# Kernel optimization log

Hardware: AMD Instinct MI355X
Metric: run time of the kernel (lower is better)

The kernel has to match this reference:

```python
import jax, jax.numpy as jnp
import numpy as np

B, S, D, H = 2, 2048, 1024, 16
A = D // H
NEG = -1e9


def setup_inputs() -> dict:
    key = jax.random.key(0)
    ks = jax.random.split(key, 5)
    std = 1.0 / np.sqrt(D)
    query = jax.random.normal(ks[0], (B, S, D), dtype=jnp.float32)
    context = jax.random.normal(ks[1], (B, S, D), dtype=jnp.float32)
    Wq = jax.random.normal(ks[2], (D, D), dtype=jnp.float32) * std
    Wkv = jax.random.normal(ks[3], (2 * D, D), dtype=jnp.float32) * std
    Wout = jax.random.normal(ks[4], (D, D), dtype=jnp.float32) * std
    # 2D additive causal mask [q_len, c_len]; module broadcasts it over batch and heads
    mask = jnp.where(jnp.tril(jnp.ones((S, S), dtype=bool)), 0.0, NEG).astype(jnp.float32)
    return {"query": query, "context": context, "Wq": Wq, "Wkv": Wkv, "Wout": Wout, "mask": mask}


def reference(query, context, Wq, Wkv, Wout, mask):
    b, q_len, d = query.shape
    c_len = context.shape[1]
    h, a = H, A
    scale = 1.0 / np.sqrt(d)  # NOTE: module scales by 1/sqrt(hidden_dim), not head dim

    q = query @ Wq.T                      # [b, q, d]
    kv = context @ Wkv.T                  # [b, c, 2d]
    k, v = jnp.split(kv, 2, axis=-1)

    q = q.reshape(b, q_len, h, a)
    k = k.reshape(b, c_len, h, a)
    v = v.reshape(b, c_len, h, a)

    scores = jnp.einsum('bqha,bkha->bqkh', q, k)      # [b, q, k, h]
    scores = scores + mask[None, :, :, None]          # mask added BEFORE scaling (faithful)
    attn = jax.nn.softmax(scores * scale, axis=2)     # softmax over key dim
    out = jnp.einsum('bqkh,bkha->bqha', attn, v).reshape(b, q_len, d)
    return out @ Wout.T
```

## Files before the change

### kernel.cpp

```cpp
#include <hip/hip_runtime.h>
#include <hip/hip_bf16.h>
#include <stdint.h>

#define S_LEN 2048
#define DIM   1024
#define NH    16
#define HD    64
#define BATCH 2

typedef __attribute__((ext_vector_type(4))) float f32x4;
typedef __attribute__((ext_vector_type(16))) float f32x16;
typedef __attribute__((ext_vector_type(8))) short bf16x8;
typedef __attribute__((ext_vector_type(4))) int i32x4;
typedef __hip_bfloat16 bf16;

__device__ inline void gload_lds16(const void* g, void* l) {
  __builtin_amdgcn_global_load_lds(
      (const __attribute__((address_space(1))) void*)g,
      (__attribute__((address_space(3))) void*)l, 16, 0, 0);
}

__device__ inline bf16x8 as_bf16x8(i32x4 x) {
  union { i32x4 i; bf16x8 v; } u; u.i = x; return u.v;
}
__device__ inline int cvt_pk_bf16(float lo, float hi) {
  int r;
  asm("v_cvt_pk_bf16_f32 %0, %1, %2" : "=v"(r) : "v"(lo), "v"(hi));
  return r;
}
__device__ inline float b2f(short s) {
  union { unsigned int u; float f; } w;
  w.u = ((unsigned int)(unsigned short)s) << 16;
  return w.f;
}

__global__ __launch_bounds__(256) void cvt_all(
    const float* __restrict__ q, const float* __restrict__ c,
    const float* __restrict__ wq, const float* __restrict__ wkv,
    const float* __restrict__ wo,
    bf16* __restrict__ oq, bf16* __restrict__ oc, bf16* __restrict__ owq,
    bf16* __restrict__ owkv, bf16* __restrict__ owo) {
  const int N0 = 1048576, N1 = 1048576, N2 = 262144, N3 = 524288, N4 = 262144;
  const int total = N0 + N1 + N2 + N3 + N4;
  for (int i = blockIdx.x * 256 + threadIdx.x; i < total; i += gridDim.x * 256) {
    const float* src; bf16* dst; int off = i;
    if (i < N0)                { src = q;   dst = oq; }
    else if (i < N0 + N1)      { src = c;   dst = oc;   off -= N0; }
    else if (i < N0 + N1 + N2) { src = wq;  dst = owq;  off -= N0 + N1; }
    else if (i < N0 + N1 + N2 + N3) { src = wkv; dst = owkv; off -= N0 + N1 + N2; }
    else                       { src = wo;  dst = owo;  off -= N0 + N1 + N2 + N3; }
    float4 v = ((const float4*)src)[off];
    bf16 b0 = __float2bfloat16(v.x), b1 = __float2bfloat16(v.y);
    bf16 b2 = __float2bfloat16(v.z), b3 = __float2bfloat16(v.w);
    ushort4 o;
    o.x = *(unsigned short*)&b0; o.y = *(unsigned short*)&b1;
    o.z = *(unsigned short*)&b2; o.w = *(unsigned short*)&b3;
    ((ushort4*)dst)[off] = o;
  }
}

__device__ inline void gemm128_core(const bf16* __restrict__ A, const bf16* __restrict__ B,
                                    int K, int bm, int bn,
                                    bf16 (*Als)[4096], bf16 (*Bls)[4096],
                                    f32x4 acc[4][4]) {
  const int tid = threadIdx.x;
  const int lane = tid & 63, wid = tid >> 6;
  const int wr = wid >> 1, wc = wid & 1;
  const int fr = lane & 15, fq = lane >> 4;
  const int nt = K >> 5;

  auto stage = [&](int buf, int kt) {
    const int k0 = kt << 5;
#pragma unroll
    for (int j = 0; j < 2; ++j) {
      int ob = wid * 2048 + j * 1024;
      int o = ob + lane * 16;
      int r = o >> 6;
      int kk = (o & 63) >> 1;
      gload_lds16(A + (size_t)(bm + r) * K + k0 + kk, (char*)Als[buf] + ob);
      gload_lds16(B + (size_t)(bn + r) * K + k0 + kk, (char*)Bls[buf] + ob);
    }
  };

  stage(0, 0);
  stage(1, 1);

  for (int i = 0; i < nt; ++i) {
    if (i + 1 < nt) asm volatile("s_waitcnt vmcnt(4)" ::: "memory");
    else            asm volatile("s_waitcnt vmcnt(0)" ::: "memory");
    __builtin_amdgcn_s_barrier();
    __builtin_amdgcn_sched_barrier(0);

    const int cb = i % 3;
    bf16x8 af[4], bfr[4];
#pragma unroll
    for (int m = 0; m < 4; ++m)
      af[m] = *(const bf16x8*)(Als[cb] + (wr * 64 + m * 16 + fr) * 32 + fq * 8);
#pragma unroll
    for (int n = 0; n < 4; ++n)
      bfr[n] = *(const bf16x8*)(Bls[cb] + (wc * 64 + n * 16 + fr) * 32 + fq * 8);
    __builtin_amdgcn_s_setprio(1);
#pragma unroll
    for (int m = 0; m < 4; ++m)
#pragma unroll
      for (int n = 0; n < 4; ++n)
        acc[m][n] = __builtin_amdgcn_mfma_f32_16x16x32_bf16(af[m], bfr[n], acc[m][n], 0, 0, 0);
    __builtin_amdgcn_s_setprio(0);

    if (i + 2 < nt) stage((i + 2) % 3, i + 2);
  }
}

__global__ __launch_bounds__(256) void gemm_proj(
    const bf16* __restrict__ Aq, const bf16* __restrict__ Bq, bf16* __restrict__ Cq,
    const bf16* __restrict__ Akv, const bf16* __restrict__ Bkv, bf16* __restrict__ Ckv,
    bf16* __restrict__ Vt, float qalpha) {
  __shared__ __align__(16) bf16 shmem[6 * 4096];
  bf16 (*Als)[4096] = (bf16(*)[4096])shmem;
  bf16 (*Bls)[4096] = (bf16(*)[4096])(shmem + 3 * 4096);

  const int bid0 = blockIdx.x;
  const int bid = (bid0 & 7) * 96 + (bid0 >> 3);
  const bf16 *A, *B; bf16 *C; int N; float alpha; int bx, by;
  if (bid < 256) { A = Aq;  B = Bq;  C = Cq;  N = 1024; alpha = qalpha; bx = bid & 7;  by = bid >> 3; }
  else { int t = bid - 256; A = Akv; B = Bkv; C = Ckv; N = 2048; alpha = 1.0f; bx = t & 15; by = t >> 4; }
  const bool vtmode = (bid >= 256) && (bx >= 8);
  const int bm = by * 128, bn = bx * 128;

  f32x4 acc[4][4] = {};
  gemm128_core(A, B, 1024, bm, bn, Als, Bls, acc);

  const int tid = threadIdx.x;
  const int lane = tid & 63, wid = tid >> 6;
  const int wr = wid >> 1, wc = wid & 1;
  const int fr = lane & 15, fq = lane >> 4;

  if (!vtmode) {
#pragma unroll
    for (int m = 0; m < 4; ++m)
#pragma unroll
      for (int n = 0; n < 4; ++n)
#pragma unroll
        for (int i = 0; i < 4; ++i) {
          int row = bm + wr * 64 + m * 16 + fq * 4 + i;
          int col = bn + wc * 64 + n * 16 + fr;
          C[(size_t)row * N + col] = __float2bfloat16(acc[m][n][i] * alpha);
        }
  } else {
    const int TP = 136;
    __syncthreads();
#pragma unroll
    for (int m = 0; m < 4; ++m)
#pragma unroll
      for (int n = 0; n < 4; ++n) {
        int tcol = wc * 64 + n * 16 + fr;
#pragma unroll
        for (int i = 0; i < 4; ++i) {
          int trow = wr * 64 + m * 16 + fq * 4 + i;
          shmem[tcol * TP + trow] = __float2bfloat16(acc[m][n][i]);
        }
      }
    __syncthreads();
    const int bb = bm >> 11, s0 = bm & 2047;
    const int vtrow0 = bb * 1024 + (bn - 1024);
#pragma unroll
    for (int j = 0; j < 8; ++j) {
      int ar = (tid >> 4) + j * 16;
      int sc = (tid & 15) * 8;
      bf16x8 v = *(const bf16x8*)&shmem[ar * TP + sc];
      *(bf16x8*)(Vt + (size_t)(vtrow0 + ar) * S_LEN + s0 + sc) = v;
    }
  }
}

__global__ __launch_bounds__(256) void gemm_bt_n64(
    const bf16* __restrict__ A, const bf16* __restrict__ B,
    float* __restrict__ C, int M, int N, int K) {
  __shared__ __align__(16) bf16 Als[3][128 * 32];
  __shared__ __align__(16) bf16 Bls[3][64 * 32];
  const int tid = threadIdx.x;
  const int lane = tid & 63, wid = tid >> 6;
  const int bid0 = blockIdx.x;
  const int bid = (bid0 & 7) * 64 + (bid0 >> 3);
  const int bx = bid & 15, by = bid >> 4;
  const int bm = by * 128, bn = bx * 64;
  const int fr = lane & 15, fq = lane >> 4;

  f32x4 acc[2][4] = {};
  const int nt = K >> 5;

  auto stage = [&](int buf, int kt) {
    const int k0 = kt << 5;
#pragma unroll
    for (int j = 0; j < 2; ++j) {
      int ob = wid * 2048 + j * 1024;
      int o = ob + lane * 16;
      int r = o >> 6;
      int kk = (o & 63) >> 1;
      gload_lds16(A + (size_t)(bm + r) * K + k0 + kk, (char*)Als[buf] + ob);
    }
    {
      int ob = wid * 1024;
      int o = ob + lane * 16;
      int r = o >> 6;
      int kk = (o & 63) >> 1;
      gload_lds16(B + (size_t)(bn + r) * K + k0 + kk, (char*)Bls[buf] + ob);
    }
  };

  stage(0, 0);
  stage(1, 1);

  for (int i = 0; i < nt; ++i) {
    if (i + 1 < nt) asm volatile("s_waitcnt vmcnt(3)" ::: "memory");
    else            asm volatile("s_waitcnt vmcnt(0)" ::: "memory");
    __builtin_amdgcn_s_barrier();
    __builtin_amdgcn_sched_barrier(0);

    const int cb = i % 3;
    bf16x8 af[2], bfr[4];
#pragma unroll
    for (int m = 0; m < 2; ++m)
      af[m] = *(const bf16x8*)(Als[cb] + (wid * 32 + m * 16 + fr) * 32 + fq * 8);
#pragma unroll
    for (int n = 0; n < 4; ++n)
      bfr[n] = *(const bf16x8*)(Bls[cb] + (n * 16 + fr) * 32 + fq * 8);
    __builtin_amdgcn_s_setprio(1);
#pragma unroll
    for (int m = 0; m < 2; ++m)
#pragma unroll
      for (int n = 0; n < 4; ++n)
        acc[m][n] = __builtin_amdgcn_mfma_f32_16x16x32_bf16(af[m], bfr[n], acc[m][n], 0, 0, 0);
    __builtin_amdgcn_s_setprio(0);

    if (i + 2 < nt) stage((i + 2) % 3, i + 2);
  }

#pragma unroll
  for (int m = 0; m < 2; ++m)
#pragma unroll
    for (int n = 0; n < 4; ++n)
#pragma unroll
      for (int i = 0; i < 4; ++i) {
        int row = bm + wid * 32 + m * 16 + fq * 4 + i;
        int col = bn + n * 16 + fr;
        C[(size_t)row * N + col] = acc[m][n][i];
      }
}

__global__ __launch_bounds__(256, 4) void attn_fwd(
    const bf16* __restrict__ Q,
    const bf16* __restrict__ KV,
    const bf16* __restrict__ Vt,
    bf16* __restrict__ Opart,
    float* __restrict__ Rpart) {
  __shared__ __align__(16) bf16 Kls[3][64 * 64];
  __shared__ __align__(16) bf16 Vls[3][64 * 64];
  const int tid = threadIdx.x, lane = tid & 63, wid = tid >> 6;
  const int l31 = lane & 31, hi = lane >> 5;
  const int bid = blockIdx.x;
  const int qx = 15 - (bid >> 6);
  const int rem = bid & 63;
  const int c = rem >> 5;
  const int hb = rem & 31;
  const int h = hb >> 1, b = hb & 1;
  const int rw0 = qx * 128 + wid * 32;
  const int qrow = rw0 + l31;
  const float NEGINF = -__builtin_inff();

  const int cnt = qx + 1;
  const int kt0 = c * cnt;
  const int p = ((b * NH + h) * 32) + qx * 2 + c;

  bf16x8 qf[4];
#pragma unroll
  for (int ka = 0; ka < 4; ++ka)
    qf[ka] = *(const bf16x8*)(Q + (size_t)(b * S_LEN + qrow) * DIM + h * HD + ka * 16 + hi * 8);

  f32x16 oacc[2] = {};
  float rsA[4] = {0.f, 0.f, 0.f, 0.f};

  const bf16* kA[2]; const bf16* vA[2]; int obA[2];
#pragma unroll
  for (int j = 0; j < 2; ++j) {
    int ob = (wid * 2 + j) * 1024;
    int o = ob + lane * 16;
    int r = o >> 7;
    int sb = (o & 127) ^ ((r & 7) << 4);
    kA[j] = KV + (size_t)(b * S_LEN + r) * (2 * DIM) + h * HD + (sb >> 1);
    vA[j] = Vt + (size_t)((b * NH + h) * HD + r) * S_LEN + (sb >> 1);
    obA[j] = ob;
  }
  const size_t kStep = (size_t)64 * 2 * DIM;
  auto stage = [&](int buf, int kt) {
#pragma unroll
    for (int j = 0; j < 2; ++j) {
      gload_lds16(kA[j] + (size_t)kt * kStep, (char*)Kls[buf] + obA[j]);
      gload_lds16(vA[j] + (size_t)kt * 64, (char*)Vls[buf] + obA[j]);
    }
  };

  stage(0, kt0);
  if (cnt > 1) stage(1, kt0 + 1);

  for (int i = 0; i < cnt; ++i) {
    const int kt = kt0 + i;
    if (i + 1 < cnt) asm volatile("s_waitcnt vmcnt(4)" ::: "memory");
    else             asm volatile("s_waitcnt vmcnt(0)" ::: "memory");
    __builtin_amdgcn_s_barrier();
    __builtin_amdgcn_sched_barrier(0);

    const int cb = i % 3;
    if (64 * kt <= rw0 + 31) {
      const bf16* Kb = Kls[cb];
      const bf16* Vb = Vls[cb];
      const bool maskt = (64 * kt + 63 > rw0);

#pragma unroll
      for (int kb = 0; kb < 2; ++kb) {
        f32x16 cc = {};
        __builtin_amdgcn_s_setprio(1);
#pragma unroll
        for (int ka = 0; ka < 4; ++ka) {
          int row = kb * 32 + l31;
          bf16x8 kf = *(const bf16x8*)((const char*)Kb + row * 128 +
                                       ((ka * 32 + hi * 16) ^ ((row & 7) << 4)));
          cc = __builtin_amdgcn_mfma_f32_32x32x16_bf16(kf, qf[ka], cc, 0, 0, 0);
        }
        __builtin_amdgcn_s_setprio(0);

        float pe[16];
        if (maskt) {
#pragma unroll
          for (int r = 0; r < 16; ++r) {
            int key = kt * 64 + kb * 32 + (r & 3) + 8 * (r >> 2) + 4 * hi;
            float s = (key <= qrow) ? cc[r] : NEGINF;
            pe[r] = __builtin_amdgcn_exp2f(s);
            rsA[r & 3] += pe[r];
          }
        } else {
#pragma unroll
          for (int r = 0; r < 16; ++r) {
            pe[r] = __builtin_amdgcn_exp2f(cc[r]);
            rsA[r & 3] += pe[r];
          }
        }

        int u0 = cvt_pk_bf16(pe[0], pe[1]),  u1 = cvt_pk_bf16(pe[2], pe[3]);
        int u2 = cvt_pk_bf16(pe[4], pe[5]),  u3 = cvt_pk_bf16(pe[6], pe[7]);
        int u4 = cvt_pk_bf16(pe[8], pe[9]),  u5 = cvt_pk_bf16(pe[10], pe[11]);
        int u6 = cvt_pk_bf16(pe[12], pe[13]), u7 = cvt_pk_bf16(pe[14], pe[15]);
        asm("v_permlane32_swap_b32 %0, %1" : "+v"(u0), "+v"(u2));
        asm("v_permlane32_swap_b32 %0, %1" : "+v"(u1), "+v"(u3));
        asm("v_permlane32_swap_b32 %0, %1" : "+v"(u4), "+v"(u6));
        asm("v_permlane32_swap_b32 %0, %1" : "+v"(u5), "+v"(u7));
        i32x4 w0, w1;
        w0[0] = u0; w0[1] = u1; w0[2] = u2; w0[3] = u3;
        w1[0] = u4; w1[1] = u5; w1[2] = u6; w1[3] = u7;
        bf16x8 pa0 = as_bf16x8(w0), pa1 = as_bf16x8(w1);

        __builtin_amdgcn_s_setprio(1);
#pragma unroll
        for (int pl = 0; pl < 2; ++pl) {
          bf16x8 pa = pl ? pa1 : pa0;
#pragma unroll
          for (int nb = 0; nb < 2; ++nb) {
            int a = nb * 32 + l31;
            bf16x8 vf = *(const bf16x8*)((const char*)Vb + a * 128 +
                                         ((kb * 64 + pl * 32 + hi * 16) ^ ((a & 7) << 4)));
            oacc[nb] = __builtin_amdgcn_mfma_f32_32x32x16_bf16(pa, vf, oacc[nb], 0, 0, 0);
          }
        }
        __builtin_amdgcn_s_setprio(0);
      }
    }

    if (i + 2 < cnt) stage((i + 2) % 3, kt0 + i + 2);
  }

  float rsum = (rsA[0] + rsA[1]) + (rsA[2] + rsA[3]);
  rsum += __shfl_xor(rsum, 32);
  if (hi == 0) Rpart[p * 128 + wid * 32 + l31] = rsum;
#pragma unroll
  for (int nb = 0; nb < 2; ++nb)
#pragma unroll
    for (int r = 0; r < 16; ++r) {
      int qloc = (r & 3) + 8 * (r >> 2) + 4 * hi;
      Opart[(size_t)p * 8192 + (wid * 32 + qloc) * 64 + nb * 32 + l31] =
          __float2bfloat16(oacc[nb][r]);
    }
}

__global__ __launch_bounds__(256) void attn_combine(
    const bf16* __restrict__ Opart, const float* __restrict__ Rpart,
    bf16* __restrict__ O) {
  const int g = blockIdx.x;
  const int qx = g & 15, bh = g >> 4;
  const int h = bh & 15, b = bh >> 4;
  const int t = threadIdx.x;
  const int row = t >> 1, col0 = (t & 1) * 32;
  const int p0 = bh * 32 + qx * 2;
  const size_t o0 = (size_t)p0 * 8192 + row * 64 + col0;
  const float rinv = 1.0f / (Rpart[p0 * 128 + row] + Rpart[p0 * 128 + 128 + row]);
  const int s = qx * 128 + row;
  bf16* dst = O + (size_t)(b * S_LEN + s) * DIM + h * HD + col0;
#pragma unroll
  for (int j = 0; j < 4; ++j) {
    bf16x8 a = *(const bf16x8*)(Opart + o0 + j * 8);
    bf16x8 cc = *(const bf16x8*)(Opart + o0 + 8192 + j * 8);
    bf16x8 w;
#pragma unroll
    for (int e = 0; e < 8; ++e) {
      bf16 r = __float2bfloat16((b2f(a[e]) + b2f(cc[e])) * rinv);
      ((short*)&w)[e] = *(short*)&r;
    }
    *(bf16x8*)(dst + j * 8) = w;
  }
}

extern "C" void kernel_launch(void* const* d_in, const int* in_sizes, int n_in,
                              void* d_out, int out_size, void* d_ws, size_t ws_size,
                              hipStream_t stream) {
  (void)in_sizes; (void)n_in; (void)out_size; (void)ws_size;
  const float* query   = (const float*)d_in[0];
  const float* context = (const float*)d_in[1];
  const float* Wq      = (const float*)d_in[2];
  const float* Wkv     = (const float*)d_in[3];
  const float* Wout    = (const float*)d_in[4];
  float* out = (float*)d_out;

  bf16* ws = (bf16*)d_ws;
  const size_t nBSD = (size_t)BATCH * S_LEN * DIM;
  bf16* qbf    = ws;
  bf16* cbf    = qbf + nBSD;
  bf16* wqbf   = cbf + nBSD;
  bf16* wkvbf  = wqbf + (size_t)DIM * DIM;
  bf16* woutbf = wkvbf + (size_t)2 * DIM * DIM;
  bf16* Qp     = woutbf + (size_t)DIM * DIM;
  bf16* KVp    = Qp + nBSD;
  bf16* Vtp    = KVp + 2 * nBSD;
  bf16* Op     = Vtp + nBSD;
  bf16*  Opart = qbf;
  float* Rpart = (float*)wqbf;

  cvt_all<<<2048, 256, 0, stream>>>(query, context, Wq, Wkv, Wout,
                                    qbf, cbf, wqbf, wkvbf, woutbf);

  gemm_proj<<<768, 256, 0, stream>>>(qbf, wqbf, Qp, cbf, wkvbf, KVp, Vtp,
                                     0.0450842200277801f);

  attn_fwd<<<1024, 256, 0, stream>>>(Qp, KVp, Vtp, Opart, Rpart);
  attn_combine<<<512, 256, 0, stream>>>(Opart, Rpart, Op);
  const int M = BATCH * S_LEN;
  gemm_bt_n64<<<512, 256, 0, stream>>>(Op, woutbf, out, M, DIM, DIM);
}
```

Before: 103.5 us.

## Fuse split-KV attention combine into output projection GEMM A-operand load

Removes the separate attn_combine kernel. The output GEMM now loads the two partial attention outputs per tile directly from global memory into registers, sums them, scales by the reciprocal row sum precomputed into LDS, and writes the bf16 result into a double-buffered A tile. This drops one launch and the round trip of the combined O tensor through memory. In exchange the A operand goes through registers instead of direct-to-LDS loads, and each of the 16 column blocks re-reads and recombines the same partials, which adds redundant loads and ALU work inside the GEMM pipeline.

```diff
diff --git a/kernel.cpp b/kernel.cpp
--- a/kernel.cpp
+++ b/kernel.cpp
@@ -173,11 +173,16 @@
   }
 }
 
-__global__ __launch_bounds__(256) void gemm_bt_n64(
-    const bf16* __restrict__ A, const bf16* __restrict__ B,
-    float* __restrict__ C, int M, int N, int K) {
-  __shared__ __align__(16) bf16 Als[3][128 * 32];
+struct ASet { bf16x8 a0, b0, a1, b1; };
+
+__global__ __launch_bounds__(256) void gemm_out_fused(
+    const bf16* __restrict__ Opart,
+    const float* __restrict__ Rpart,
+    const bf16* __restrict__ B,
+    float* __restrict__ C) {
+  __shared__ __align__(16) bf16 Als[2][128 * 32];
   __shared__ __align__(16) bf16 Bls[3][64 * 32];
+  __shared__ float Rls[2048];
   const int tid = threadIdx.x;
   const int lane = tid & 63, wid = tid >> 6;
   const int bid0 = blockIdx.x;
@@ -185,43 +190,68 @@
   const int bx = bid & 15, by = bid >> 4;
   const int bm = by * 128, bn = bx * 64;
   const int fr = lane & 15, fq = lane >> 4;
+  const int b = by >> 4, qx = by & 15;
+  const int K = 1024, nt = 32;
+
+#pragma unroll
+  for (int it = 0; it < 8; ++it) {
+    int idx = tid + it * 256;
+    int hh = idx >> 7, rt = idx & 127;
+    int pp = (b * 16 + hh) * 32 + qx * 2;
+    Rls[idx] = 1.0f / (Rpart[pp * 128 + rt] + Rpart[pp * 128 + 128 + rt]);
+  }
+  __syncthreads();
+
+  const int rj0 = wid * 32 + (lane >> 2);
+  const int kk = (lane & 3) * 8;
+  const int offA0 = rj0 * 64 + kk;
+  const int offA1 = offA0 + 1024;
+  const int wb0 = wid * 2048 + lane * 16;
+  const int wb1 = wb0 + 1024;
+  const size_t pstride = 8192;
+
+  auto pbase = [&](int kt) -> size_t {
+    int hh = kt >> 1;
+    return (size_t)((b * 16 + hh) * 32 + qx * 2) * pstride + (kt & 1) * 32;
+  };
+  auto issueA = [&](ASet& s, int kt) {
+    const bf16* pa = Opart + pbase(kt);
+    s.a0 = *(const bf16x8*)(pa + offA0);
+    s.b0 = *(const bf16x8*)(pa + offA0 + pstride);
+    s.a1 = *(const bf16x8*)(pa + offA1);
+    s.b1 = *(const bf16x8*)(pa + offA1 + pstride);
+  };
+  auto gloadB = [&](int buf, int kt) {
+    const int k0 = kt << 5;
+    int ob = wid * 1024;
+    int o = ob + lane * 16;
+    int r = o >> 6;
+    int kb = (o & 63) >> 1;
+    gload_lds16(B + (size_t)(bn + r) * K + k0 + kb, (char*)Bls[buf] + ob);
+  };
+  auto writeA = [&](int buf, const ASet& s, int kt) {
+    int hh = kt >> 1;
+    float rv0 = Rls[hh * 128 + rj0];
+    float rv1 = Rls[hh * 128 + rj0 + 16];
+    i32x4 w;
+    w[0] = cvt_pk_bf16((b2f(s.a0[0]) + b2f(s.b0[0])) * rv0, (b2f(s.a0[1]) + b2f(s.b0[1])) * rv0);
+    w[1] = cvt_pk_bf16((b2f(s.a0[2]) + b2f(s.b0[2])) * rv0, (b2f(s.a0[3]) + b2f(s.b0[3])) * rv0);
+    w[2] = cvt_pk_bf16((b2f(s.a0[4]) + b2f(s.b0[4])) * rv0, (b2f(s.a0[5]) + b2f(s.b0[5])) * rv0);
+    w[3] = cvt_pk_bf16((b2f(s.a0[6]) + b2f(s.b0[6])) * rv0, (b2f(s.a0[7]) + b2f(s.b0[7])) * rv0);
+    *(i32x4*)((char*)Als[buf] + wb0) = w;
+    w[0] = cvt_pk_bf16((b2f(s.a1[0]) + b2f(s.b1[0])) * rv1, (b2f(s.a1[1]) + b2f(s.b1[1])) * rv1);
+    w[1] = cvt_pk_bf16((b2f(s.a1[2]) + b2f(s.b1[2])) * rv1, (b2f(s.a1[3]) + b2f(s.b1[3])) * rv1);
+    w[2] = cvt_pk_bf16((b2f(s.a1[4]) + b2f(s.b1[4])) * rv1, (b2f(s.a1[5]) + b2f(s.b1[5])) * rv1);
+    w[3] = cvt_pk_bf16((b2f(s.a1[6]) + b2f(s.b1[6])) * rv1, (b2f(s.a1[7]) + b2f(s.b1[7])) * rv1);
+    *(i32x4*)((char*)Als[buf] + wb1) = w;
+  };
 
   f32x4 acc[2][4] = {};
-  const int nt = K >> 5;
-
-  auto stage = [&](int buf, int kt) {
-    const int k0 = kt << 5;
-#pragma unroll
-    for (int j = 0; j < 2; ++j) {
-      int ob = wid * 2048 + j * 1024;
-      int o = ob + lane * 16;
-      int r = o >> 6;
-      int kk = (o & 63) >> 1;
-      gload_lds16(A + (size_t)(bm + r) * K + k0 + kk, (char*)Als[buf] + ob);
-    }
-    {
-      int ob = wid * 1024;
-      int o = ob + lane * 16;
-      int r = o >> 6;
-      int kk = (o & 63) >> 1;
-      gload_lds16(B + (size_t)(bn + r) * K + k0 + kk, (char*)Bls[buf] + ob);
-    }
-  };
-
-  stage(0, 0);
-  stage(1, 1);
-
-  for (int i = 0; i < nt; ++i) {
-    if (i + 1 < nt) asm volatile("s_waitcnt vmcnt(3)" ::: "memory");
-    else            asm volatile("s_waitcnt vmcnt(0)" ::: "memory");
-    __builtin_amdgcn_s_barrier();
-    __builtin_amdgcn_sched_barrier(0);
-
-    const int cb = i % 3;
+  auto compute = [&](int abuf, int cb) {
     bf16x8 af[2], bfr[4];
 #pragma unroll
     for (int m = 0; m < 2; ++m)
-      af[m] = *(const bf16x8*)(Als[cb] + (wid * 32 + m * 16 + fr) * 32 + fq * 8);
+      af[m] = *(const bf16x8*)(Als[abuf] + (wid * 32 + m * 16 + fr) * 32 + fq * 8);
 #pragma unroll
     for (int n = 0; n < 4; ++n)
       bfr[n] = *(const bf16x8*)(Bls[cb] + (n * 16 + fr) * 32 + fq * 8);
@@ -232,8 +262,44 @@
       for (int n = 0; n < 4; ++n)
         acc[m][n] = __builtin_amdgcn_mfma_f32_16x16x32_bf16(af[m], bfr[n], acc[m][n], 0, 0, 0);
     __builtin_amdgcn_s_setprio(0);
-
-    if (i + 2 < nt) stage((i + 2) % 3, i + 2);
+  };
+
+  ASet sA, sB;
+  issueA(sA, 0); gloadB(0, 0);
+  issueA(sB, 1); gloadB(1, 1);
+  asm volatile("s_waitcnt vmcnt(5)" ::: "memory");
+  writeA(0, sA, 0);
+  asm volatile("s_waitcnt lgkmcnt(0)" ::: "memory");
+  __builtin_amdgcn_s_barrier();
+  __builtin_amdgcn_sched_barrier(0);
+
+  for (int i0 = 0; i0 < nt; i0 += 2) {
+    {
+      const int i = i0;
+      compute(0, i % 3);
+      if (i + 2 < nt) { issueA(sA, i + 2); gloadB((i + 2) % 3, i + 2); }
+      if (i + 1 < nt) {
+        if (i + 2 < nt) asm volatile("s_waitcnt vmcnt(5)" ::: "memory");
+        else            asm volatile("s_waitcnt vmcnt(0)" ::: "memory");
+        writeA(1, sB, i + 1);
+        asm volatile("s_waitcnt lgkmcnt(0)" ::: "memory");
+        __builtin_amdgcn_s_barrier();
+        __builtin_amdgcn_sched_barrier(0);
+      }
+    }
+    {
+      const int i = i0 + 1;
+      compute(1, i % 3);
+      if (i + 2 < nt) { issueA(sB, i + 2); gloadB((i + 2) % 3, i + 2); }
+      if (i + 1 < nt) {
+        if (i + 2 < nt) asm volatile("s_waitcnt vmcnt(5)" ::: "memory");
+        else            asm volatile("s_waitcnt vmcnt(0)" ::: "memory");
+        writeA(0, sA, i + 1);
+        asm volatile("s_waitcnt lgkmcnt(0)" ::: "memory");
+        __builtin_amdgcn_s_barrier();
+        __builtin_amdgcn_sched_barrier(0);
+      }
+    }
   }
 
 #pragma unroll
@@ -244,7 +310,7 @@
       for (int i = 0; i < 4; ++i) {
         int row = bm + wid * 32 + m * 16 + fq * 4 + i;
         int col = bn + n * 16 + fr;
-        C[(size_t)row * N + col] = acc[m][n][i];
+        C[(size_t)row * 1024 + col] = acc[m][n][i];
       }
 }
 
@@ -391,33 +457,6 @@
     }
 }
 
-__global__ __launch_bounds__(256) void attn_combine(
-    const bf16* __restrict__ Opart, const float* __restrict__ Rpart,
-    bf16* __restrict__ O) {
-  const int g = blockIdx.x;
-  const int qx = g & 15, bh = g >> 4;
-  const int h = bh & 15, b = bh >> 4;
-  const int t = threadIdx.x;
-  const int row = t >> 1, col0 = (t & 1) * 32;
-  const int p0 = bh * 32 + qx * 2;
-  const size_t o0 = (size_t)p0 * 8192 + row * 64 + col0;
-  const float rinv = 1.0f / (Rpart[p0 * 128 + row] + Rpart[p0 * 128 + 128 + row]);
-  const int s = qx * 128 + row;
-  bf16* dst = O + (size_t)(b * S_LEN + s) * DIM + h * HD + col0;
-#pragma unroll
-  for (int j = 0; j < 4; ++j) {
-    bf16x8 a = *(const bf16x8*)(Opart + o0 + j * 8);
-    bf16x8 cc = *(const bf16x8*)(Opart + o0 + 8192 + j * 8);
-    bf16x8 w;
-#pragma unroll
-    for (int e = 0; e < 8; ++e) {
-      bf16 r = __float2bfloat16((b2f(a[e]) + b2f(cc[e])) * rinv);
-      ((short*)&w)[e] = *(short*)&r;
-    }
-    *(bf16x8*)(dst + j * 8) = w;
-  }
-}
-
 extern "C" void kernel_launch(void* const* d_in, const int* in_sizes, int n_in,
                               void* d_out, int out_size, void* d_ws, size_t ws_size,
                               hipStream_t stream) {
@@ -439,7 +478,6 @@
   bf16* Qp     = woutbf + (size_t)DIM * DIM;
   bf16* KVp    = Qp + nBSD;
   bf16* Vtp    = KVp + 2 * nBSD;
-  bf16* Op     = Vtp + nBSD;
   bf16*  Opart = qbf;
   float* Rpart = (float*)wqbf;
 
@@ -450,7 +488,6 @@
                                      0.0450842200277801f);
 
   attn_fwd<<<1024, 256, 0, stream>>>(Qp, KVp, Vtp, Opart, Rpart);
-  attn_combine<<<512, 256, 0, stream>>>(Opart, Rpart, Op);
-  const int M = BATCH * S_LEN;
-  gemm_bt_n64<<<512, 256, 0, stream>>>(Op, woutbf, out, M, DIM, DIM);
-}
+
+  gemm_out_fused<<<512, 256, 0, stream>>>(Opart, Rpart, woutbf, out);
+}
```

Measured after the change: 106.9 us. 3.3% more time.
